# Kernel optimization log

Measured on AMD Instinct MI355X. Metric: run time of the kernel, lower is better.

The kernel has to match this reference:

```python
import jax, jax.numpy as jnp
import numpy as np
from jax import lax

BS, N, MAXITER = 64, 1024, 50


def setup_inputs() -> dict:
    key = jax.random.key(0)
    kA, kb, kM = jax.random.split(key, 3)
    B = jax.random.normal(kA, (BS, N, N), dtype=jnp.float32)
    # SPD system matrix: A = B B^T / N + I  (well-conditioned for CG)
    A = B @ jnp.swapaxes(B, -1, -2) / N + jnp.eye(N, dtype=jnp.float32)
    b = jax.random.normal(kb, (BS, N, 1), dtype=jnp.float32)
    x0 = jnp.zeros((BS, N, 1), dtype=jnp.float32)
    # learned preconditioner M_inv: positive diagonal (SPD)
    d = 1.0 + jax.random.uniform(kM, (BS, N), dtype=jnp.float32)
    M_inv = jax.vmap(jnp.diag)(d)
    rtol = jnp.zeros((BS,), dtype=jnp.float32)
    return {"A": A, "b": b, "x0": x0, "M_inv": M_inv, "rtol": rtol, "maxiter": MAXITER}


def reference(A, b, x0, M_inv, rtol, maxiter):
    # Batched preconditioned CG. history: (bs, maxiter+1) residual norms.
    def bdot(u, v):  # batched inner product -> (bs,1,1)
        return jnp.sum(u * v, axis=(1, 2), keepdims=True)

    r0 = b - A @ x0                       # (bs,n,1)
    z0 = M_inv @ r0
    rnorm0 = jnp.sqrt(jnp.sum(r0 * r0, axis=(1, 2)))  # (bs,)

    def step(carry, _):
        x, r, z, p = carry
        Ap = A @ p
        rz = bdot(r, z)
        alpha = rz / bdot(p, Ap)
        x = x + alpha * p
        r_new = r - alpha * Ap
        z_new = M_inv @ r_new
        beta = bdot(r_new, z_new) / rz
        p = z_new + beta * p
        rnorm = jnp.sqrt(jnp.sum(r_new * r_new, axis=(1, 2)))
        return (x, r_new, z_new, p), rnorm

    _, hist = lax.scan(step, (x0, r0, z0, z0), None, length=maxiter)
    # hist: (maxiter, bs) -> stack with initial norm -> (bs, maxiter+1)
    return jnp.concatenate([rnorm0[:, None], hist.T], axis=1)
```

## Files before the change

### kernel.cpp

```cpp
#include <hip/hip_runtime.h>
#include <math.h>

#define BS 64
#define N 1024
#define NCHUNK 16
#define CCOLS 64
#define THREADS 256
#define LGRP 8
#define MAXITER 50
#define OUTW (MAXITER + 1)

typedef _Float16 half4 __attribute__((ext_vector_type(4)));


__device__ inline float wave_reduce(float v) {
#pragma unroll
    for (int off = 32; off > 0; off >>= 1) v += __shfl_xor(v, off, 64);
    return v;
}

__device__ inline float block_reduce1(float a, float* red, int lane, int wave) {
    a = wave_reduce(a);
    if (lane == 0) red[wave] = a;
    __syncthreads();
    return red[0] + red[1] + red[2] + red[3];
}

__device__ inline float2 block_reduce2(float a, float b, float* redA,
                                       float* redB, int lane, int wave) {
    a = wave_reduce(a);
    b = wave_reduce(b);
    if (lane == 0) {
        redA[wave] = a;
        redB[wave] = b;
    }
    __syncthreads();
    float2 r;
    r.x = redA[0] + redA[1] + redA[2] + redA[3];
    r.y = redB[0] + redB[1] + redB[2] + redB[3];
    return r;
}

__device__ inline void panel_store(float4 acc, float* wredf, float* ydst,
                                   int tid) {
    acc.x += __shfl_xor(acc.x, 16, 64); acc.x += __shfl_xor(acc.x, 32, 64);
    acc.y += __shfl_xor(acc.y, 16, 64); acc.y += __shfl_xor(acc.y, 32, 64);
    acc.z += __shfl_xor(acc.z, 16, 64); acc.z += __shfl_xor(acc.z, 32, 64);
    acc.w += __shfl_xor(acc.w, 16, 64); acc.w += __shfl_xor(acc.w, 32, 64);
    const int lane = tid & 63;
    const int wave = tid >> 6;
    if (lane < 16) {
        float* w4 = wredf + wave * 64 + lane * 4;
        w4[0] = acc.x; w4[1] = acc.y; w4[2] = acc.z; w4[3] = acc.w;
    }
    __syncthreads();
    if (tid < CCOLS)
        ydst[tid] =
            wredf[tid] + wredf[64 + tid] + wredf[128 + tid] + wredf[192 + tid];
}

__global__ __launch_bounds__(THREADS, 4) void l0_kernel(
    const float* __restrict__ A, const float* __restrict__ x0,
    const float* __restrict__ Minv, _Float16* __restrict__ Ah,
    float* __restrict__ yv, float* __restrict__ dv) {
    const int batch = blockIdx.x >> 4;
    const int chunk = blockIdx.x & 15;
    const int c0 = chunk * CCOLS;
    const int tid = threadIdx.x;

    __shared__ float p_lds[N];
    __shared__ float wredf[256];

    const size_t vb = (size_t)batch * N;
    ((float4*)p_lds)[tid] = ((const float4*)(x0 + vb))[tid];
    if (tid < CCOLS)
        dv[vb + c0 + tid] =
            Minv[(size_t)batch * N * N + (size_t)(c0 + tid) * (N + 1)];
    __syncthreads();

    const int rg = tid >> 4;
    const int cq4 = (c0 >> 2) + (tid & 15);
    const float4* __restrict__ Af = (const float4*)(A + (size_t)batch * N * N);
    half4* __restrict__ Ah4 = (half4*)(Ah + (size_t)batch * N * N);
    float4 acc = {0.f, 0.f, 0.f, 0.f};
#pragma unroll 1
    for (int sb = 0; sb < 64; sb += LGRP) {
        float4 av[LGRP];
#pragma unroll
        for (int u = 0; u < LGRP; ++u)
            av[u] = Af[(size_t)(rg + 16 * (sb + u)) * (N / 4) + cq4];
#pragma unroll
        for (int u = 0; u < LGRP; ++u) {
            half4 h;
            h[0] = (_Float16)av[u].x; h[1] = (_Float16)av[u].y;
            h[2] = (_Float16)av[u].z; h[3] = (_Float16)av[u].w;
            Ah4[(size_t)(rg + 16 * (sb + u)) * (N / 4) + cq4] = h;
            const float pj = p_lds[rg + 16 * (sb + u)];
            acc.x += (float)h[0] * pj; acc.y += (float)h[1] * pj;
            acc.z += (float)h[2] * pj; acc.w += (float)h[3] * pj;
        }
    }
    panel_store(acc, wredf, yv + vb + c0, tid);
}

__global__ __launch_bounds__(THREADS, 4) void iter_kernel(
    const _Float16* __restrict__ Ah, const float* __restrict__ bvec,
    const float* __restrict__ dv, float* __restrict__ yv,
    float* __restrict__ rv2, float* __restrict__ pv2,
    float* __restrict__ rzs2, float* __restrict__ out, int k) {
    const int batch = blockIdx.x >> 4;
    const int chunk = blockIdx.x & 15;
    const int c0 = chunk * CCOLS;
    const int tid = threadIdx.x;
    const int lane = tid & 63;
    const int wave = tid >> 6;

    __shared__ float p_lds[N];
    __shared__ float wredf[256];
    __shared__ float redP[4], redA[4], redB[4];

    const int ro = (k - 1) & 1;
    const int wo = k & 1;
    const size_t vb = (size_t)batch * N;
    const size_t vro = (size_t)ro * BS * N + vb;
    const size_t vwo = (size_t)wo * BS * N + vb;

    float4 y4 = ((const float4*)(yv + vro))[tid];
    float4 dd = ((const float4*)(dv + vb))[tid];
    float4 rr, pp;
    float rz_new, rn;
    if (k == 1) {
        float4 b4 = ((const float4*)(bvec + vb))[tid];
        rr.x = b4.x - y4.x; rr.y = b4.y - y4.y;
        rr.z = b4.z - y4.z; rr.w = b4.w - y4.w;
        pp.x = dd.x * rr.x; pp.y = dd.y * rr.y;
        pp.z = dd.z * rr.z; pp.w = dd.w * rr.w;
        float lrz = rr.x * pp.x + rr.y * pp.y + rr.z * pp.z + rr.w * pp.w;
        float lrn = rr.x * rr.x + rr.y * rr.y + rr.z * rr.z + rr.w * rr.w;
        float2 s = block_reduce2(lrz, lrn, redA, redB, lane, wave);
        rz_new = s.x; rn = s.y;
    } else {
        float4 p4 = ((const float4*)(pv2 + vro))[tid];
        rr = ((const float4*)(rv2 + vro))[tid];
        const float rzp = rzs2[ro * BS + batch];
        float lpap = p4.x * y4.x + p4.y * y4.y + p4.z * y4.z + p4.w * y4.w;
        float pap = block_reduce1(lpap, redP, lane, wave);
        float alpha = rzp / pap;
        rr.x -= alpha * y4.x; rr.y -= alpha * y4.y;
        rr.z -= alpha * y4.z; rr.w -= alpha * y4.w;
        float4 zz;
        zz.x = dd.x * rr.x; zz.y = dd.y * rr.y;
        zz.z = dd.z * rr.z; zz.w = dd.w * rr.w;
        float lrz = rr.x * zz.x + rr.y * zz.y + rr.z * zz.z + rr.w * zz.w;
        float lrn = rr.x * rr.x + rr.y * rr.y + rr.z * rr.z + rr.w * rr.w;
        float2 s = block_reduce2(lrz, lrn, redA, redB, lane, wave);
        rz_new = s.x; rn = s.y;
        float beta = rz_new / rzp;
        pp.x = zz.x + beta * p4.x; pp.y = zz.y + beta * p4.y;
        pp.z = zz.z + beta * p4.z; pp.w = zz.w + beta * p4.w;
    }
    if (chunk == 0) {
        ((float4*)(rv2 + vwo))[tid] = rr;
        ((float4*)(pv2 + vwo))[tid] = pp;
        if (tid == 0) {
            rzs2[wo * BS + batch] = rz_new;
            out[batch * OUTW + (k - 1)] = sqrtf(rn);
        }
    }
    ((float4*)p_lds)[tid] = pp;
    __syncthreads();

    const int rg = tid >> 4;
    const int cq4 = (c0 >> 2) + (tid & 15);
    const half4* __restrict__ A4 = (const half4*)(Ah + (size_t)batch * N * N);
    float4 acc = {0.f, 0.f, 0.f, 0.f};
#pragma unroll 1
    for (int sb = 0; sb < 64; sb += LGRP) {
        half4 a[LGRP];
#pragma unroll
        for (int u = 0; u < LGRP; ++u)
            a[u] = A4[(size_t)(rg + 16 * (sb + u)) * (N / 4) + cq4];
#pragma unroll
        for (int u = 0; u < LGRP; ++u) {
            const float pj = p_lds[rg + 16 * (sb + u)];
            acc.x += (float)a[u][0] * pj;
            acc.y += (float)a[u][1] * pj;
            acc.z += (float)a[u][2] * pj;
            acc.w += (float)a[u][3] * pj;
        }
    }
    panel_store(acc, wredf, yv + vwo + c0, tid);
}

__global__ __launch_bounds__(THREADS) void final_kernel(
    const float* __restrict__ yv, const float* __restrict__ pv2,
    const float* __restrict__ rv2, const float* __restrict__ rzs2,
    float* __restrict__ out) {
    const int batch = blockIdx.x;
    const int tid = threadIdx.x;
    const int lane = tid & 63;
    const int wave = tid >> 6;
    __shared__ float redP[4], redA[4];

    const size_t vb = (size_t)batch * N;
    float4 y4 = ((const float4*)(yv + vb))[tid];
    float4 p4 = ((const float4*)(pv2 + vb))[tid];
    float4 rr = ((const float4*)(rv2 + vb))[tid];
    const float rzp = rzs2[batch];
    float lpap = p4.x * y4.x + p4.y * y4.y + p4.z * y4.z + p4.w * y4.w;
    float pap = block_reduce1(lpap, redP, lane, wave);
    float alpha = rzp / pap;
    rr.x -= alpha * y4.x; rr.y -= alpha * y4.y;
    rr.z -= alpha * y4.z; rr.w -= alpha * y4.w;
    float lrn = rr.x * rr.x + rr.y * rr.y + rr.z * rr.z + rr.w * rr.w;
    float rn = block_reduce1(lrn, redA, lane, wave);
    if (tid == 0) out[batch * OUTW + MAXITER] = sqrtf(rn);
}

extern "C" void kernel_launch(void* const* d_in, const int* in_sizes, int n_in,
                              void* d_out, int out_size, void* d_ws,
                              size_t ws_size, hipStream_t stream) {
    (void)in_sizes; (void)n_in; (void)out_size; (void)ws_size;
    const float* A = (const float*)d_in[0];
    const float* b = (const float*)d_in[1];
    const float* x0 = (const float*)d_in[2];
    const float* Minv = (const float*)d_in[3];
    float* out = (float*)d_out;

    _Float16* Ah = (_Float16*)d_ws;
    float* yv = (float*)(Ah + (size_t)BS * N * N);
    float* rv2 = yv + (size_t)2 * BS * N;
    float* pv2 = rv2 + (size_t)2 * BS * N;
    float* dv = pv2 + (size_t)2 * BS * N;
    float* rzs2 = dv + (size_t)BS * N;

    dim3 blk(THREADS);
    l0_kernel<<<BS * NCHUNK, blk, 0, stream>>>(A, x0, Minv, Ah, yv, dv);
    for (int k = 1; k <= MAXITER; ++k)
        iter_kernel<<<BS * NCHUNK, blk, 0, stream>>>(Ah, b, dv, yv, rv2, pv2,
                                                     rzs2, out, k);
    final_kernel<<<BS, blk, 0, stream>>>(yv, pv2, rv2, rzs2, out);
}
```

Before: 1.565 ms.

## Prefetch first A tiles before CG reductions and double-buffer matvec loads

In the per-iteration kernel, the first two groups of fp16 A rows are now loaded before the vector update and block reductions, so global memory latency overlaps the alpha/beta computation. The matvec loop is restructured into a software-pipelined double buffer of 4-row groups that prefetches the next two groups while accumulating the current ones. The chunk-0 state writes move after the matvec. This raises register pressure (16 half4 buffers live at once) under a 4-block occupancy bound, which could cause spills or lower occupancy.

```diff
diff --git a/kernel.cpp b/kernel.cpp
--- a/kernel.cpp
+++ b/kernel.cpp
@@ -6,7 +6,8 @@
 #define NCHUNK 16
 #define CCOLS 64
 #define THREADS 256
-#define LGRP 8
+#define LGRP 4
+#define NGRP 16
 #define MAXITER 50
 #define OUTW (MAXITER + 1)
 
@@ -84,13 +85,13 @@
     half4* __restrict__ Ah4 = (half4*)(Ah + (size_t)batch * N * N);
     float4 acc = {0.f, 0.f, 0.f, 0.f};
 #pragma unroll 1
-    for (int sb = 0; sb < 64; sb += LGRP) {
-        float4 av[LGRP];
-#pragma unroll
-        for (int u = 0; u < LGRP; ++u)
+    for (int sb = 0; sb < 64; sb += 8) {
+        float4 av[8];
+#pragma unroll
+        for (int u = 0; u < 8; ++u)
             av[u] = Af[(size_t)(rg + 16 * (sb + u)) * (N / 4) + cq4];
 #pragma unroll
-        for (int u = 0; u < LGRP; ++u) {
+        for (int u = 0; u < 8; ++u) {
             half4 h;
             h[0] = (_Float16)av[u].x; h[1] = (_Float16)av[u].y;
             h[2] = (_Float16)av[u].z; h[3] = (_Float16)av[u].w;
@@ -125,12 +126,31 @@
     const size_t vro = (size_t)ro * BS * N + vb;
     const size_t vwo = (size_t)wo * BS * N + vb;
 
+    const int rg = tid >> 4;
+    const int cq4 = (c0 >> 2) + (tid & 15);
+    const half4* __restrict__ A4 = (const half4*)(Ah + (size_t)batch * N * N);
+#define AIDX(g, u) ((size_t)(rg + 16 * (LGRP * (g) + (u))) * (N / 4) + cq4)
+
     float4 y4 = ((const float4*)(yv + vro))[tid];
     float4 dd = ((const float4*)(dv + vb))[tid];
-    float4 rr, pp;
+    float4 p4 = {0.f, 0.f, 0.f, 0.f};
+    float4 rr = {0.f, 0.f, 0.f, 0.f};
+    float4 b4 = {0.f, 0.f, 0.f, 0.f};
+    if (k == 1) {
+        b4 = ((const float4*)(bvec + vb))[tid];
+    } else {
+        p4 = ((const float4*)(pv2 + vro))[tid];
+        rr = ((const float4*)(rv2 + vro))[tid];
+    }
+    half4 bufA[LGRP], bufB[LGRP];
+#pragma unroll
+    for (int u = 0; u < LGRP; ++u) bufA[u] = A4[AIDX(0, u)];
+#pragma unroll
+    for (int u = 0; u < LGRP; ++u) bufB[u] = A4[AIDX(1, u)];
+
+    float4 pp;
     float rz_new, rn;
     if (k == 1) {
-        float4 b4 = ((const float4*)(bvec + vb))[tid];
         rr.x = b4.x - y4.x; rr.y = b4.y - y4.y;
         rr.z = b4.z - y4.z; rr.w = b4.w - y4.w;
         pp.x = dd.x * rr.x; pp.y = dd.y * rr.y;
@@ -140,8 +160,6 @@
         float2 s = block_reduce2(lrz, lrn, redA, redB, lane, wave);
         rz_new = s.x; rn = s.y;
     } else {
-        float4 p4 = ((const float4*)(pv2 + vro))[tid];
-        rr = ((const float4*)(rv2 + vro))[tid];
         const float rzp = rzs2[ro * BS + batch];
         float lpap = p4.x * y4.x + p4.y * y4.y + p4.z * y4.z + p4.w * y4.w;
         float pap = block_reduce1(lpap, redP, lane, wave);
@@ -159,6 +177,55 @@
         pp.x = zz.x + beta * p4.x; pp.y = zz.y + beta * p4.y;
         pp.z = zz.z + beta * p4.z; pp.w = zz.w + beta * p4.w;
     }
+    ((float4*)p_lds)[tid] = pp;
+    __syncthreads();
+
+    float4 acc = {0.f, 0.f, 0.f, 0.f};
+#pragma unroll 1
+    for (int g = 0; g + 2 < NGRP; g += 2) {
+        half4 nA[LGRP], nB[LGRP];
+#pragma unroll
+        for (int u = 0; u < LGRP; ++u) nA[u] = A4[AIDX(g + 2, u)];
+#pragma unroll
+        for (int u = 0; u < LGRP; ++u) nB[u] = A4[AIDX(g + 3, u)];
+#pragma unroll
+        for (int u = 0; u < LGRP; ++u) {
+            const float pj = p_lds[rg + 16 * (LGRP * g + u)];
+            acc.x += (float)bufA[u][0] * pj;
+            acc.y += (float)bufA[u][1] * pj;
+            acc.z += (float)bufA[u][2] * pj;
+            acc.w += (float)bufA[u][3] * pj;
+        }
+#pragma unroll
+        for (int u = 0; u < LGRP; ++u) {
+            const float pj = p_lds[rg + 16 * (LGRP * (g + 1) + u)];
+            acc.x += (float)bufB[u][0] * pj;
+            acc.y += (float)bufB[u][1] * pj;
+            acc.z += (float)bufB[u][2] * pj;
+            acc.w += (float)bufB[u][3] * pj;
+        }
+#pragma unroll
+        for (int u = 0; u < LGRP; ++u) { bufA[u] = nA[u]; bufB[u] = nB[u]; }
+    }
+#pragma unroll
+    for (int u = 0; u < LGRP; ++u) {
+        const float pj = p_lds[rg + 16 * (LGRP * (NGRP - 2) + u)];
+        acc.x += (float)bufA[u][0] * pj;
+        acc.y += (float)bufA[u][1] * pj;
+        acc.z += (float)bufA[u][2] * pj;
+        acc.w += (float)bufA[u][3] * pj;
+    }
+#pragma unroll
+    for (int u = 0; u < LGRP; ++u) {
+        const float pj = p_lds[rg + 16 * (LGRP * (NGRP - 1) + u)];
+        acc.x += (float)bufB[u][0] * pj;
+        acc.y += (float)bufB[u][1] * pj;
+        acc.z += (float)bufB[u][2] * pj;
+        acc.w += (float)bufB[u][3] * pj;
+    }
+#undef AIDX
+    panel_store(acc, wredf, yv + vwo + c0, tid);
+
     if (chunk == 0) {
         ((float4*)(rv2 + vwo))[tid] = rr;
         ((float4*)(pv2 + vwo))[tid] = pp;
@@ -167,29 +234,6 @@
             out[batch * OUTW + (k - 1)] = sqrtf(rn);
         }
     }
-    ((float4*)p_lds)[tid] = pp;
-    __syncthreads();
-
-    const int rg = tid >> 4;
-    const int cq4 = (c0 >> 2) + (tid & 15);
-    const half4* __restrict__ A4 = (const half4*)(Ah + (size_t)batch * N * N);
-    float4 acc = {0.f, 0.f, 0.f, 0.f};
-#pragma unroll 1
-    for (int sb = 0; sb < 64; sb += LGRP) {
-        half4 a[LGRP];
-#pragma unroll
-        for (int u = 0; u < LGRP; ++u)
-            a[u] = A4[(size_t)(rg + 16 * (sb + u)) * (N / 4) + cq4];
-#pragma unroll
-        for (int u = 0; u < LGRP; ++u) {
-            const float pj = p_lds[rg + 16 * (sb + u)];
-            acc.x += (float)a[u][0] * pj;
-            acc.y += (float)a[u][1] * pj;
-            acc.z += (float)a[u][2] * pj;
-            acc.w += (float)a[u][3] * pj;
-        }
-    }
-    panel_store(acc, wredf, yv + vwo + c0, tid);
 }
 
 __global__ __launch_bounds__(THREADS) void final_kernel(
```

After: 1.554 ms, median of 2. About the same (-0.7%).
